# Kernel optimization log

Measured on AMD Instinct MI355X. Metric: run time of the kernel, lower is better.

The kernel has to match this reference:

```python
import jax, jax.numpy as jnp
import numpy as np

R_ROT = 6   # rotation order R
r = 7       # icosahedral resolution
H, W = 2 ** r, 2 ** (r + 1)


def _reorder_idx(r, R):
    """Flat gather indices implementing FlatPadIco boundary stitching."""
    H, W = 2 ** r, 2 ** (r + 1)
    idx_in = np.arange(R * 5 * H * W, dtype=np.int64).reshape(R, 5, H, W)
    idx_out = np.zeros((R, 5, H + 2, W + 2), dtype=np.int64)
    idx_out[..., 1:-1, 1:-1] = idx_in
    idx_out[..., 0, 1:2 ** r + 1] = np.roll(idx_in, 1, -3)[..., -1, 2 ** r:]
    idx_out[..., 0, 2 ** r + 1:-1] = np.roll(np.roll(idx_in, 1, -3), -1, -4)[..., :, -1][..., ::-1]
    idx_out[..., -1, 2:2 ** r + 2] = np.roll(np.roll(idx_in, -1, -3), -1, -4)[..., :, 0][..., ::-1]
    idx_out[..., -1, 2 ** r + 1:-1] = np.roll(idx_in, -1, -3)[..., 0, 0:2 ** r]
    idx_out[..., 1:-1, 0] = np.roll(np.roll(idx_in, 1, -3), 1, -4)[..., -1, 0:2 ** r][..., ::-1]
    idx_out[..., 2:, -1] = np.roll(np.roll(idx_in, -1, -3), 1, -4)[..., 0, 2 ** r:][..., ::-1]
    return idx_out


def _neighbor_idx(r):
    """7-neighbor (hex) indices into the padded (H+2, W+2) charts."""
    dh = np.array([0, 1, 1, 0, -1, -1, 0], dtype=np.int64)
    dw = np.array([0, 0, 1, 1, 0, -1, -1], dtype=np.int64)
    h = np.arange(2 ** (r - 1), dtype=np.int64)
    w = np.arange(2 ** r, dtype=np.int64)
    nh = 1 + 2 * h[:, None, None] + dh[None, None, :]   # (H/2, 1, 7)
    nw = 1 + 2 * w[None, :, None] + dw[None, None, :]   # (1, W/2, 7)
    shape = (2 ** (r - 1), 2 ** r, 7)
    return np.broadcast_to(nh, shape).copy(), np.broadcast_to(nw, shape).copy()


def _clean_mask(rr):
    """CleanVertices mask: zero the two pole pixels of each chart."""
    m = np.ones((2 ** rr, 2 ** (rr + 1)), dtype=np.float32)
    m[-1, 0] = 0.0   # north pole vertex
    m[0, -1] = 0.0   # south pole vertex
    return m


_RIDX = jnp.asarray(_reorder_idx(r, R_ROT))
_NH, _NW = (jnp.asarray(a) for a in _neighbor_idx(r))
_MASK_IN = jnp.asarray(_clean_mask(r))
_MASK_OUT = jnp.asarray(_clean_mask(r - 1))


def setup_inputs() -> dict:
    key = jax.random.key(0)
    x = jax.random.normal(key, (4, 16, R_ROT, 5, H, W), dtype=jnp.float32)
    return {"x": x}


def reference(x) -> jnp.ndarray:
    # CleanVertices(r) inside FlatPadIco
    x = x * _MASK_IN
    # FlatPadIco: flatten (R, charts, H, W) and gather with stitched indices
    xf = x.reshape(x.shape[:-4] + (-1,))          # (..., R*5*H*W)
    y = xf[..., _RIDX]                            # (..., R, 5, H+2, W+2)
    # 7-neighbor gather + mean pooling
    rf = y[..., _NH, _NW]                         # (..., R, 5, H/2, W/2, 7)
    out = jnp.mean(rf, axis=-1)                   # (..., R, 5, H/2, W/2)
    # CleanVertices(r-1) on pooled output
    return out * _MASK_OUT
```

## Files before the change

### kernel.cpp

```cpp
#include <hip/hip_runtime.h>


#define WW 256

__global__ __launch_bounds__(256) void flat_pool_ico(const float* __restrict__ x,
                                                     float* __restrict__ out) {
    int t = blockIdx.x * 256 + threadIdx.x;
    int lane = t & 31;
    int rowid = t >> 5;
    int h = rowid & 63;
    int tmp = rowid >> 6;
    int c = tmp % 5; tmp /= 5;
    int rot = tmp % 6;
    int b = tmp / 6;
    int w0 = lane << 2;
    int cm = w0 << 1;

    int slab = (b * 6 + rot) * 5 + c;
    const float* xs   = x + ((long)slab << 15);
    const float* rowm = xs + (h << 9);
    const float* rowb = rowm + WW;

    float mid[9];
    float top[8];
    float bot[8];

    {
        float4 a0 = *(const float4*)(rowm + cm);
        float4 a1 = *(const float4*)(rowm + cm + 4);
        mid[1]=a0.x; mid[2]=a0.y; mid[3]=a0.z; mid[4]=a0.w;
        mid[5]=a1.x; mid[6]=a1.y; mid[7]=a1.z; mid[8]=a1.w;
        float4 b0 = *(const float4*)(rowb + cm);
        float4 b1 = *(const float4*)(rowb + cm + 4);
        bot[0]=b0.x; bot[1]=b0.y; bot[2]=b0.z; bot[3]=b0.w;
        bot[4]=b1.x; bot[5]=b1.y; bot[6]=b1.z; bot[7]=b1.w;
    }

    int cprev = (c + 4) % 5;

    if (lane == 0) {
        const float* xn3 = x + ((long)((b * 6 + (rot + 5) % 6) * 5 + cprev) << 15) + 127 * WW;
        mid[0] = xn3[127 - (h << 1)];
    } else {
        mid[0] = rowm[cm - 1];
    }

    if (h == 0) {
        const float* xn1 = x + ((long)((b * 6 + rot) * 5 + cprev) << 15) + 127 * WW + 127;
        const float* xn2 = x + ((long)((b * 6 + (rot + 1) % 6) * 5 + cprev) << 15) + 255;
        #pragma unroll
        for (int i = 0; i < 8; ++i) {
            int pw = cm + i;
            float v;
            if (pw == 0)        v = x[(long)b * 983040];
            else if (pw <= 128) v = xn1[pw];
            else                v = xn2[(256 - pw) << 8];
            top[i] = v;
        }
    } else {
        const float* rowt = rowm - WW;
        float4 t0v = *(const float4*)(rowt + cm);
        float4 t1v = *(const float4*)(rowt + cm + 4);
        top[1]=t0v.x; top[2]=t0v.y; top[3]=t0v.z; top[4]=t0v.w;
        top[5]=t1v.x; top[6]=t1v.y; top[7]=t1v.z;
        if (lane == 0) {
            const float* xn3 = x + ((long)((b * 6 + (rot + 5) % 6) * 5 + cprev) << 15) + 127 * WW;
            top[0] = xn3[128 - (h << 1)];
        } else {
            top[0] = rowt[cm - 1];
        }
    }

    const float inv7 = 1.0f / 7.0f;
    float o[4];
    #pragma unroll
    for (int k = 0; k < 4; ++k) {
        float s = mid[2*k] + mid[2*k+1] + mid[2*k+2]
                + top[2*k] + top[2*k+1]
                + bot[2*k] + bot[2*k+1];
        o[k] = s * inv7;
    }

    if (h == 63 && lane == 0)  o[0] = 0.0f;
    if (h == 0  && lane == 31) o[3] = 0.0f;

    float* op = out + ((long)slab << 13) + (h << 7) + w0;
    *(float4*)op = make_float4(o[0], o[1], o[2], o[3]);
}

extern "C" void kernel_launch(void* const* d_in, const int* in_sizes, int n_in,
                              void* d_out, int out_size, void* d_ws, size_t ws_size,
                              hipStream_t stream) {
    const float* x = (const float*)d_in[0];
    float* out = (float*)d_out;
    flat_pool_ico<<<15360, 256, 0, stream>>>(x, out);
}
```

Before: 71.18 us.

## Double outputs per thread, share left halo via shuffles, use nontemporal stores

Each thread now computes 8 pooled outputs instead of 4, halving the grid and loading 16-wide row segments. The left-neighbour element of the middle and top rows now comes from the adjacent lane via __shfl_up instead of a separate unaligned global load. Output writes use nontemporal stores. The intent is fewer scalar loads and less per-thread index overhead. The cost is more registers per thread and fewer resident threads to hide memory latency.

```diff
diff --git a/kernel.cpp b/kernel.cpp
--- a/kernel.cpp
+++ b/kernel.cpp
@@ -3,89 +3,101 @@
 
 #define WW 256
 
+typedef float vfloat4 __attribute__((ext_vector_type(4)));
+
 __global__ __launch_bounds__(256) void flat_pool_ico(const float* __restrict__ x,
                                                      float* __restrict__ out) {
     int t = blockIdx.x * 256 + threadIdx.x;
-    int lane = t & 31;
-    int rowid = t >> 5;
+    int lane = t & 15;
+    int rowid = t >> 4;
     int h = rowid & 63;
     int tmp = rowid >> 6;
     int c = tmp % 5; tmp /= 5;
     int rot = tmp % 6;
     int b = tmp / 6;
-    int w0 = lane << 2;
+    int w0 = lane << 3;
     int cm = w0 << 1;
 
-    int slab = (b * 6 + rot) * 5 + c;
-    const float* xs   = x + ((long)slab << 15);
+    long slab = (long)((b * 6 + rot) * 5 + c);
+    const float* xs   = x + (slab << 15);
     const float* rowm = xs + (h << 9);
     const float* rowb = rowm + WW;
 
-    float mid[9];
-    float top[8];
-    float bot[8];
+    float M[17], T[16], B[16];
 
     {
-        float4 a0 = *(const float4*)(rowm + cm);
-        float4 a1 = *(const float4*)(rowm + cm + 4);
-        mid[1]=a0.x; mid[2]=a0.y; mid[3]=a0.z; mid[4]=a0.w;
-        mid[5]=a1.x; mid[6]=a1.y; mid[7]=a1.z; mid[8]=a1.w;
-        float4 b0 = *(const float4*)(rowb + cm);
-        float4 b1 = *(const float4*)(rowb + cm + 4);
-        bot[0]=b0.x; bot[1]=b0.y; bot[2]=b0.z; bot[3]=b0.w;
-        bot[4]=b1.x; bot[5]=b1.y; bot[6]=b1.z; bot[7]=b1.w;
+        vfloat4 a0 = *(const vfloat4*)(rowm + cm);
+        vfloat4 a1 = *(const vfloat4*)(rowm + cm + 4);
+        vfloat4 a2 = *(const vfloat4*)(rowm + cm + 8);
+        vfloat4 a3 = *(const vfloat4*)(rowm + cm + 12);
+        M[1]=a0.x;  M[2]=a0.y;  M[3]=a0.z;  M[4]=a0.w;
+        M[5]=a1.x;  M[6]=a1.y;  M[7]=a1.z;  M[8]=a1.w;
+        M[9]=a2.x;  M[10]=a2.y; M[11]=a2.z; M[12]=a2.w;
+        M[13]=a3.x; M[14]=a3.y; M[15]=a3.z; M[16]=a3.w;
+        vfloat4 c0 = *(const vfloat4*)(rowb + cm);
+        vfloat4 c1 = *(const vfloat4*)(rowb + cm + 4);
+        vfloat4 c2 = *(const vfloat4*)(rowb + cm + 8);
+        vfloat4 c3 = *(const vfloat4*)(rowb + cm + 12);
+        B[0]=c0.x;  B[1]=c0.y;  B[2]=c0.z;  B[3]=c0.w;
+        B[4]=c1.x;  B[5]=c1.y;  B[6]=c1.z;  B[7]=c1.w;
+        B[8]=c2.x;  B[9]=c2.y;  B[10]=c2.z; B[11]=c2.w;
+        B[12]=c3.x; B[13]=c3.y; B[14]=c3.z; B[15]=c3.w;
     }
 
     int cprev = (c + 4) % 5;
+    const float* xn3 = x + ((long)((b * 6 + (rot + 5) % 6) * 5 + cprev) << 15) + 127 * WW;
 
-    if (lane == 0) {
-        const float* xn3 = x + ((long)((b * 6 + (rot + 5) % 6) * 5 + cprev) << 15) + 127 * WW;
-        mid[0] = xn3[127 - (h << 1)];
-    } else {
-        mid[0] = rowm[cm - 1];
+    {
+        float midL = __shfl_up(M[16], 1);
+        if (lane == 0) midL = xn3[127 - (h << 1)];
+        M[0] = midL;
     }
 
     if (h == 0) {
         const float* xn1 = x + ((long)((b * 6 + rot) * 5 + cprev) << 15) + 127 * WW + 127;
         const float* xn2 = x + ((long)((b * 6 + (rot + 1) % 6) * 5 + cprev) << 15) + 255;
         #pragma unroll
-        for (int i = 0; i < 8; ++i) {
+        for (int i = 0; i < 16; ++i) {
             int pw = cm + i;
             float v;
             if (pw == 0)        v = x[(long)b * 983040];
             else if (pw <= 128) v = xn1[pw];
             else                v = xn2[(256 - pw) << 8];
-            top[i] = v;
+            T[i] = v;
         }
     } else {
         const float* rowt = rowm - WW;
-        float4 t0v = *(const float4*)(rowt + cm);
-        float4 t1v = *(const float4*)(rowt + cm + 4);
-        top[1]=t0v.x; top[2]=t0v.y; top[3]=t0v.z; top[4]=t0v.w;
-        top[5]=t1v.x; top[6]=t1v.y; top[7]=t1v.z;
-        if (lane == 0) {
-            const float* xn3 = x + ((long)((b * 6 + (rot + 5) % 6) * 5 + cprev) << 15) + 127 * WW;
-            top[0] = xn3[128 - (h << 1)];
-        } else {
-            top[0] = rowt[cm - 1];
-        }
+        vfloat4 t0 = *(const vfloat4*)(rowt + cm);
+        vfloat4 t1 = *(const vfloat4*)(rowt + cm + 4);
+        vfloat4 t2 = *(const vfloat4*)(rowt + cm + 8);
+        vfloat4 t3 = *(const vfloat4*)(rowt + cm + 12);
+        T[1]=t0.x;  T[2]=t0.y;  T[3]=t0.z;  T[4]=t0.w;
+        T[5]=t1.x;  T[6]=t1.y;  T[7]=t1.z;  T[8]=t1.w;
+        T[9]=t2.x;  T[10]=t2.y; T[11]=t2.z; T[12]=t2.w;
+        T[13]=t3.x; T[14]=t3.y; T[15]=t3.z;
+        float topL = __shfl_up(t3.w, 1);
+        if (lane == 0) topL = xn3[128 - (h << 1)];
+        T[0] = topL;
     }
 
     const float inv7 = 1.0f / 7.0f;
-    float o[4];
+    float o[8];
     #pragma unroll
-    for (int k = 0; k < 4; ++k) {
-        float s = mid[2*k] + mid[2*k+1] + mid[2*k+2]
-                + top[2*k] + top[2*k+1]
-                + bot[2*k] + bot[2*k+1];
+    for (int k = 0; k < 8; ++k) {
+        float s = M[2*k] + M[2*k+1] + M[2*k+2]
+                + T[2*k] + T[2*k+1]
+                + B[2*k] + B[2*k+1];
         o[k] = s * inv7;
     }
 
     if (h == 63 && lane == 0)  o[0] = 0.0f;
-    if (h == 0  && lane == 31) o[3] = 0.0f;
+    if (h == 0  && lane == 15) o[7] = 0.0f;
 
-    float* op = out + ((long)slab << 13) + (h << 7) + w0;
-    *(float4*)op = make_float4(o[0], o[1], o[2], o[3]);
+    float* op = out + (slab << 13) + (h << 7) + w0;
+    vfloat4 s0 = { o[0], o[1], o[2], o[3] };
+    vfloat4 s1 = { o[4], o[5], o[6], o[7] };
+    __builtin_nontemporal_store(s0, (vfloat4*)op);
+    __builtin_nontemporal_store(s1, (vfloat4*)(op + 4));
 }
 
 extern "C" void kernel_launch(void* const* d_in, const int* in_sizes, int n_in,
@@ -93,5 +105,5 @@
                               hipStream_t stream) {
     const float* x = (const float*)d_in[0];
     float* out = (float*)d_out;
-    flat_pool_ico<<<15360, 256, 0, stream>>>(x, out);
+    flat_pool_ico<<<7680, 256, 0, stream>>>(x, out);
 }
```

Result: faster. 58.79 us, median of 3 (-17.4%).

## Process 16 outputs per thread with wavefront shuffles and nontemporal stores

Applied to the files above, without the earlier changes.

Each thread now computes 16 pooled outputs instead of 4, so one output row is handled by 8 threads and the grid shrinks to a quarter. The left-neighbor value that used to be reloaded from global memory now comes from the previous lane with a shuffle. Outputs are written with nontemporal vector stores. This cuts redundant loads and per-thread index arithmetic, but raises register pressure and leaves fewer threads in flight to hide memory latency. The pole mask conditions are updated for the new lane count.

```diff
diff --git a/kernel.cpp b/kernel.cpp
--- a/kernel.cpp
+++ b/kernel.cpp
@@ -3,89 +3,91 @@
 
 #define WW 256
 
+typedef float vfloat4 __attribute__((ext_vector_type(4)));
+
+__device__ __forceinline__ void load32(const float* p, float* d) {
+    #pragma unroll
+    for (int q = 0; q < 8; ++q) {
+        vfloat4 v = *(const vfloat4*)(p + q * 4);
+        d[q*4+0] = v.x; d[q*4+1] = v.y; d[q*4+2] = v.z; d[q*4+3] = v.w;
+    }
+}
+
 __global__ __launch_bounds__(256) void flat_pool_ico(const float* __restrict__ x,
                                                      float* __restrict__ out) {
     int t = blockIdx.x * 256 + threadIdx.x;
-    int lane = t & 31;
-    int rowid = t >> 5;
+    int lane = t & 7;
+    int rowid = t >> 3;
     int h = rowid & 63;
     int tmp = rowid >> 6;
     int c = tmp % 5; tmp /= 5;
     int rot = tmp % 6;
     int b = tmp / 6;
-    int w0 = lane << 2;
+    int w0 = lane << 4;
     int cm = w0 << 1;
 
-    int slab = (b * 6 + rot) * 5 + c;
-    const float* xs   = x + ((long)slab << 15);
+    long slab = (long)((b * 6 + rot) * 5 + c);
+    const float* xs   = x + (slab << 15);
     const float* rowm = xs + (h << 9);
     const float* rowb = rowm + WW;
 
-    float mid[9];
-    float top[8];
-    float bot[8];
+    int cprev = (c + 4) % 5;
+    const float* xn3 = x + ((long)((b * 6 + (rot + 5) % 6) * 5 + cprev) << 15) + 127 * WW;
+
+    const float inv7 = 1.0f / 7.0f;
+    float o[16];
 
     {
-        float4 a0 = *(const float4*)(rowm + cm);
-        float4 a1 = *(const float4*)(rowm + cm + 4);
-        mid[1]=a0.x; mid[2]=a0.y; mid[3]=a0.z; mid[4]=a0.w;
-        mid[5]=a1.x; mid[6]=a1.y; mid[7]=a1.z; mid[8]=a1.w;
-        float4 b0 = *(const float4*)(rowb + cm);
-        float4 b1 = *(const float4*)(rowb + cm + 4);
-        bot[0]=b0.x; bot[1]=b0.y; bot[2]=b0.z; bot[3]=b0.w;
-        bot[4]=b1.x; bot[5]=b1.y; bot[6]=b1.z; bot[7]=b1.w;
-    }
-
-    int cprev = (c + 4) % 5;
-
-    if (lane == 0) {
-        const float* xn3 = x + ((long)((b * 6 + (rot + 5) % 6) * 5 + cprev) << 15) + 127 * WW;
-        mid[0] = xn3[127 - (h << 1)];
-    } else {
-        mid[0] = rowm[cm - 1];
+        float Mv[32], Bv[32];
+        load32(rowm + cm, Mv);
+        load32(rowb + cm, Bv);
+        float midL = __shfl_up(Mv[31], 1);
+        if (lane == 0) midL = xn3[127 - (h << 1)];
+        #pragma unroll
+        for (int k = 0; k < 16; ++k) {
+            float m0 = (k == 0) ? midL : Mv[2*k - 1];
+            float s = m0 + Mv[2*k] + Mv[2*k+1]
+                    + Bv[2*k] + Bv[2*k+1];
+            o[k] = s;
+        }
     }
 
     if (h == 0) {
         const float* xn1 = x + ((long)((b * 6 + rot) * 5 + cprev) << 15) + 127 * WW + 127;
         const float* xn2 = x + ((long)((b * 6 + (rot + 1) % 6) * 5 + cprev) << 15) + 255;
         #pragma unroll
-        for (int i = 0; i < 8; ++i) {
+        for (int i = 0; i < 32; ++i) {
             int pw = cm + i;
             float v;
             if (pw == 0)        v = x[(long)b * 983040];
             else if (pw <= 128) v = xn1[pw];
             else                v = xn2[(256 - pw) << 8];
-            top[i] = v;
+            o[i >> 1] += v;
         }
     } else {
-        const float* rowt = rowm - WW;
-        float4 t0v = *(const float4*)(rowt + cm);
-        float4 t1v = *(const float4*)(rowt + cm + 4);
-        top[1]=t0v.x; top[2]=t0v.y; top[3]=t0v.z; top[4]=t0v.w;
-        top[5]=t1v.x; top[6]=t1v.y; top[7]=t1v.z;
-        if (lane == 0) {
-            const float* xn3 = x + ((long)((b * 6 + (rot + 5) % 6) * 5 + cprev) << 15) + 127 * WW;
-            top[0] = xn3[128 - (h << 1)];
-        } else {
-            top[0] = rowt[cm - 1];
+        float Tv[32];
+        load32(rowm - WW + cm, Tv);
+        float topL = __shfl_up(Tv[31], 1);
+        if (lane == 0) topL = xn3[128 - (h << 1)];
+        #pragma unroll
+        for (int k = 0; k < 16; ++k) {
+            float t0 = (k == 0) ? topL : Tv[2*k - 1];
+            o[k] += t0 + Tv[2*k];
         }
     }
 
-    const float inv7 = 1.0f / 7.0f;
-    float o[4];
     #pragma unroll
-    for (int k = 0; k < 4; ++k) {
-        float s = mid[2*k] + mid[2*k+1] + mid[2*k+2]
-                + top[2*k] + top[2*k+1]
-                + bot[2*k] + bot[2*k+1];
-        o[k] = s * inv7;
+    for (int k = 0; k < 16; ++k) o[k] *= inv7;
+
+    if (h == 63 && lane == 0) o[0]  = 0.0f;
+    if (h == 0  && lane == 7) o[15] = 0.0f;
+
+    float* op = out + (slab << 13) + (h << 7) + w0;
+    #pragma unroll
+    for (int q = 0; q < 4; ++q) {
+        vfloat4 s = { o[q*4], o[q*4+1], o[q*4+2], o[q*4+3] };
+        __builtin_nontemporal_store(s, (vfloat4*)(op + q * 4));
     }
-
-    if (h == 63 && lane == 0)  o[0] = 0.0f;
-    if (h == 0  && lane == 31) o[3] = 0.0f;
-
-    float* op = out + ((long)slab << 13) + (h << 7) + w0;
-    *(float4*)op = make_float4(o[0], o[1], o[2], o[3]);
 }
 
 extern "C" void kernel_launch(void* const* d_in, const int* in_sizes, int n_in,
@@ -93,5 +95,5 @@
                               hipStream_t stream) {
     const float* x = (const float*)d_in[0];
     float* out = (float*)d_out;
-    flat_pool_ico<<<15360, 256, 0, stream>>>(x, out);
+    flat_pool_ico<<<3840, 256, 0, stream>>>(x, out);
 }
```

Result: slower. 79.47 us (+11.6%).
